# Performance work log

Measured on AMD Instinct MI355X. Metric: run time of the kernel, lower is better.

## Reference

```python
import jax, jax.numpy as jnp
import numpy as np

B, C, L = 8, 512, 8192
H = 8  # head_count
DK = C // H  # head key channels
DV = C // H  # head value channels


def setup_inputs() -> dict:
    key = jax.random.key(0)
    ks = jax.random.split(key, 10)
    s = 1.0 / np.sqrt(C)
    return {
        "input_": jax.random.normal(ks[0], (B, C, L), jnp.float32),
        "context_": jax.random.normal(ks[1], (B, C, L), jnp.float32),
        "Wk": jax.random.normal(ks[2], (C, C), jnp.float32) * s,
        "bk": jax.random.normal(ks[3], (C,), jnp.float32) * 0.01,
        "Wq": jax.random.normal(ks[4], (C, C), jnp.float32) * s,
        "bq": jax.random.normal(ks[5], (C,), jnp.float32) * 0.01,
        "Wv": jax.random.normal(ks[6], (C, C), jnp.float32) * s,
        "bv": jax.random.normal(ks[7], (C,), jnp.float32) * 0.01,
        "Wr": jax.random.normal(ks[8], (C, C), jnp.float32) * s,
        "br": jax.random.normal(ks[9], (C,), jnp.float32) * 0.01,
    }


def _proj(W, b, x):
    # 1x1 Conv1d == channel matmul: [O,C] x [B,C,L] -> [B,O,L]
    return jnp.einsum('oc,bcl->bol', W, x) + b[None, :, None]


def reference(input_, context_, Wk, bk, Wq, bq, Wv, bv, Wr, br):
    b, _, l = input_.shape
    keys = _proj(Wk, bk, context_).reshape(b, H, DK, l)
    queries = _proj(Wq, bq, input_).reshape(b, H, DK, l)
    values = _proj(Wv, bv, context_).reshape(b, H, DV, l)
    # per-head: softmax(K) over sequence, softmax(Q) over head-key channels
    k = jax.nn.softmax(keys, axis=3)
    q = jax.nn.softmax(queries, axis=2)
    # context = K @ V^T : [b,h,dk,dv]
    ctx = jnp.einsum('bhkl,bhvl->bhkv', k, values)
    # attended = context^T @ Q : [b,h,dv,l]
    att = jnp.einsum('bhkv,bhkl->bhvl', ctx, q).reshape(b, H * DV, l)
    return _proj(Wr, br, att) + input_
```

## Files before the change

### kernel.cpp

```cpp
#include <hip/hip_runtime.h>

#define NB 8
#define NC 512
#define NL 8192
#define NH 8
#define ND 64

typedef float f32x4 __attribute__((ext_vector_type(4)));
typedef __bf16 bf16x8 __attribute__((ext_vector_type(8)));
typedef unsigned int u32x4 __attribute__((ext_vector_type(4)));

__device__ __forceinline__ unsigned short f2bf(float f) {
    unsigned u = __builtin_bit_cast(unsigned, f);
    u += 0x7fffu + ((u >> 16) & 1u);
    return (unsigned short)(u >> 16);
}
__device__ __forceinline__ float bf2f(unsigned short s) {
    unsigned u = ((unsigned)s) << 16;
    return __builtin_bit_cast(float, u);
}
__device__ __forceinline__ float bf2f_lo(unsigned w) {
    return __builtin_bit_cast(float, w << 16);
}
__device__ __forceinline__ float bf2f_hi(unsigned w) {
    return __builtin_bit_cast(float, w & 0xffff0000u);
}
__device__ __forceinline__ bf16x8 frag_from_u32x4(u32x4 v) {
    return __builtin_bit_cast(bf16x8, v);
}
__device__ __forceinline__ bf16x8 ld_frag_lds(const unsigned short* p) {
    const unsigned* q = (const unsigned*)p;
    u32x4 v = { q[0], q[1], q[2], q[3] };
    return frag_from_u32x4(v);
}
__device__ __forceinline__ bf16x8 ld_frag_g16(const unsigned short* p) {
    return frag_from_u32x4(*(const u32x4*)p);
}

__global__ __launch_bounds__(256) void cvt_w_kernel(const float* __restrict__ s,
                                                    unsigned short* __restrict__ d, int n) {
    int i = blockIdx.x * 256 + threadIdx.x;
    if (i < n) d[i] = f2bf(s[i]);
}

__global__ __launch_bounds__(256) void zero_kernel(float* __restrict__ p, int n) {
    int i = blockIdx.x * 256 + threadIdx.x;
    if (i < n) p[i] = 0.f;
}

__global__ __launch_bounds__(256) void concat_bias_kernel(const float* __restrict__ a,
                                                          const float* __restrict__ b,
                                                          float* __restrict__ d) {
    int i = blockIdx.x * 256 + threadIdx.x;
    d[i] = (i < NC) ? a[i] : b[i - NC];
}

template<int MT, bool XBF, bool RESID, bool PERB, bool QSM>
__global__ __launch_bounds__(256) void gemm_kernel(
    const unsigned short* __restrict__ Wb,
    const void* __restrict__ Xv,
    const float* __restrict__ bias,
    const float* __restrict__ resid,
    void* __restrict__ Yv)
{
    const int bx = blockIdx.x;
    const int g  = bx >> 3;
    const int mt = g % MT;
    const int nt = (g / MT) * 8 + (bx & 7);
    const int b  = blockIdx.y;
    const int t  = threadIdx.x;
    const int wave = t >> 6, lane = t & 63;
    const int m0 = mt * 128, n0 = nt * 128;
    const int wm = (wave & 1) * 64, wn = (wave >> 1) * 64;
    const int OC = MT * 128;

    __shared__ alignas(16) unsigned short lA[128][34];
    __shared__ alignas(16) unsigned short lX[128][34];

    f32x4 acc[4][4] = {};

    const float* Xf = (const float*)Xv;
    const unsigned short* Xh = (const unsigned short*)Xv;
    const size_t xbase = (size_t)b * NC * NL;
    const unsigned short* Wp = Wb + (PERB ? (size_t)b * NC * NC : 0);

    for (int k0 = 0; k0 < NC; k0 += 32) {
        {
            int id = t;
            #pragma unroll
            for (int it = 0; it < 2; ++it, id += 256) {
                const int r = id >> 2, s = id & 3;
                u32x4 v = *(const u32x4*)(Wp + (size_t)(m0 + r) * NC + k0 + s * 8);
                unsigned* p = (unsigned*)&lA[r][s * 8];
                p[0] = v.x; p[1] = v.y; p[2] = v.z; p[3] = v.w;
            }
        }
        if constexpr (!XBF) {
            #pragma unroll
            for (int it = 0; it < 16; ++it) {
                const int kr = it * 2 + (t >> 7);
                const int l  = t & 127;
                lX[l][kr] = f2bf(Xf[xbase + (size_t)(k0 + kr) * NL + n0 + l]);
            }
        } else {
            #pragma unroll
            for (int it = 0; it < 8; ++it) {
                const int kr = it * 4 + (t >> 6);
                const int l2 = (t & 63) * 2;
                unsigned v = *(const unsigned*)(Xh + xbase + (size_t)(k0 + kr) * NL + n0 + l2);
                lX[l2][kr]     = (unsigned short)(v & 0xffffu);
                lX[l2 + 1][kr] = (unsigned short)(v >> 16);
            }
        }
        __syncthreads();

        const int koff = (lane >> 4) * 8;
        bf16x8 af[4], bfx[4];
        #pragma unroll
        for (int i = 0; i < 4; ++i)
            af[i] = ld_frag_lds(&lA[wm + i * 16 + (lane & 15)][koff]);
        #pragma unroll
        for (int j = 0; j < 4; ++j)
            bfx[j] = ld_frag_lds(&lX[wn + j * 16 + (lane & 15)][koff]);
        #pragma unroll
        for (int i = 0; i < 4; ++i)
            #pragma unroll
            for (int j = 0; j < 4; ++j)
                acc[i][j] = __builtin_amdgcn_mfma_f32_16x16x32_bf16(af[i], bfx[j], acc[i][j], 0, 0, 0);
        __syncthreads();
    }

    const int col = lane & 15, row0 = (lane >> 4) * 4;

    if constexpr (QSM) {
        #pragma unroll
        for (int i = 0; i < 4; ++i)
            #pragma unroll
            for (int r = 0; r < 4; ++r) {
                const float bo = bias[m0 + wm + i * 16 + row0 + r];
                #pragma unroll
                for (int j = 0; j < 4; ++j) acc[i][j][r] += bo;
            }
        float inv[4];
        #pragma unroll
        for (int j = 0; j < 4; ++j) {
            float m = -1e30f;
            #pragma unroll
            for (int i = 0; i < 4; ++i)
                #pragma unroll
                for (int r = 0; r < 4; ++r) m = fmaxf(m, acc[i][j][r]);
            m = fmaxf(m, __shfl_xor(m, 16));
            m = fmaxf(m, __shfl_xor(m, 32));
            float s = 0.f;
            #pragma unroll
            for (int i = 0; i < 4; ++i)
                #pragma unroll
                for (int r = 0; r < 4; ++r) {
                    const float e = __expf(acc[i][j][r] - m);
                    acc[i][j][r] = e;
                    s += e;
                }
            s += __shfl_xor(s, 16);
            s += __shfl_xor(s, 32);
            inv[j] = 1.0f / s;
        }
        unsigned short* Y = (unsigned short*)Yv;
        #pragma unroll
        for (int i = 0; i < 4; ++i)
            #pragma unroll
            for (int r = 0; r < 4; ++r) {
                const int o = m0 + wm + i * 16 + row0 + r;
                const size_t rb = (size_t)b * OC * NL + (size_t)o * NL + n0 + wn;
                #pragma unroll
                for (int j = 0; j < 4; ++j)
                    Y[rb + j * 16 + col] = f2bf(acc[i][j][r] * inv[j]);
            }
    } else {
        #pragma unroll
        for (int i = 0; i < 4; ++i) {
            #pragma unroll
            for (int r = 0; r < 4; ++r) {
                const int o = m0 + wm + i * 16 + row0 + r;
                const float bo = bias[o];
                const size_t rb = (size_t)b * OC * NL + (size_t)o * NL + n0 + wn;
                if constexpr (RESID) {
                    float* Y = (float*)Yv;
                    #pragma unroll
                    for (int j = 0; j < 4; ++j) {
                        const size_t idx = rb + j * 16 + col;
                        Y[idx] = acc[i][j][r] + bo + resid[idx];
                    }
                } else {
                    unsigned short* Y = (unsigned short*)Yv;
                    #pragma unroll
                    for (int j = 0; j < 4; ++j)
                        Y[rb + j * 16 + col] = f2bf(acc[i][j][r] + bo);
                }
            }
        }
    }
}

__global__ __launch_bounds__(256) void softmax_rows(unsigned short* __restrict__ KV) {
    const int row = blockIdx.x;
    const int t = threadIdx.x;
    const int wave = t >> 6, lane = t & 63;
    unsigned short* p = KV + ((size_t)(row >> 9) * 2 * NC + (row & 511)) * NL;

    float v[32];
    float mx = -1e30f;
    #pragma unroll
    for (int i = 0; i < 4; ++i) {
        u32x4 raw = *(const u32x4*)(p + (size_t)(i * 256 + t) * 8);
        #pragma unroll
        for (int d = 0; d < 4; ++d) {
            unsigned w = raw[d];
            v[i * 8 + d * 2]     = bf2f_lo(w);
            v[i * 8 + d * 2 + 1] = bf2f_hi(w);
        }
        #pragma unroll
        for (int j = 0; j < 8; ++j) mx = fmaxf(mx, v[i * 8 + j]);
    }
    #pragma unroll
    for (int off = 32; off > 0; off >>= 1) mx = fmaxf(mx, __shfl_down(mx, off));
    __shared__ float red[16];
    if (lane == 0) red[wave] = mx;
    __syncthreads();
    mx = fmaxf(fmaxf(red[0], red[1]), fmaxf(red[2], red[3]));

    float s = 0.f;
    #pragma unroll
    for (int i = 0; i < 32; ++i) { v[i] = __expf(v[i] - mx); s += v[i]; }
    #pragma unroll
    for (int off = 32; off > 0; off >>= 1) s += __shfl_down(s, off);
    if (lane == 0) red[8 + wave] = s;
    __syncthreads();
    s = red[8] + red[9] + red[10] + red[11];
    const float inv = 1.0f / s;

    #pragma unroll
    for (int i = 0; i < 4; ++i) {
        u32x4 outw;
        #pragma unroll
        for (int d = 0; d < 4; ++d) {
            unsigned lo = f2bf(v[i * 8 + d * 2] * inv);
            unsigned hi = f2bf(v[i * 8 + d * 2 + 1] * inv);
            outw[d] = lo | (hi << 16);
        }
        *(u32x4*)(p + (size_t)(i * 256 + t) * 8) = outw;
    }
}

__global__ __launch_bounds__(256) void ctx_kernel(
    const unsigned short* __restrict__ KV,
    float* __restrict__ ctx)
{
    const int bh = blockIdx.x;
    const int sp = blockIdx.y;
    const int t = threadIdx.x;
    const int wave = t >> 6, lane = t & 63;
    const int b = bh >> 3, h = bh & 7;
    const size_t base_k = ((size_t)b * 2 * NC + h * ND) * NL;
    const size_t base_v = base_k + (size_t)NC * NL;
    const int i = wave * 16 + (lane & 15);
    const int koff = (lane >> 4) * 8;
    const unsigned short* Ka = KV + base_k + (size_t)i * NL + koff;

    f32x4 acc[4] = {};
    const int l0 = sp * (NL / 16);
    for (int l = l0; l < l0 + (NL / 16); l += 32) {
        bf16x8 a = ld_frag_g16(Ka + l);
        #pragma unroll
        for (int j = 0; j < 4; ++j) {
            bf16x8 bv = ld_frag_g16(KV + base_v + (size_t)(j * 16 + (lane & 15)) * NL + l + koff);
            acc[j] = __builtin_amdgcn_mfma_f32_16x16x32_bf16(a, bv, acc[j], 0, 0, 0);
        }
    }
    const int col = lane & 15, row0 = (lane >> 4) * 4;
    #pragma unroll
    for (int j = 0; j < 4; ++j)
        #pragma unroll
        for (int r = 0; r < 4; ++r)
            atomicAdd(&ctx[(size_t)bh * (ND * ND) + (size_t)(wave * 16 + row0 + r) * ND + j * 16 + col],
                      acc[j][r]);
}

__global__ __launch_bounds__(512) void fold_kernel(
    const unsigned short* __restrict__ Wrb,
    const float* __restrict__ ctxb,
    unsigned short* __restrict__ Mb)
{
    const int bh = blockIdx.x;
    const int b = bh >> 3, h = bh & 7;
    const int t = threadIdx.x;
    const int wave = t >> 6, lane = t & 63;

    __shared__ unsigned short lc[64 * 66];
    const float* cs = ctxb + (size_t)bh * (ND * ND);
    #pragma unroll
    for (int it = 0; it < 8; ++it) {
        int i = it * 512 + t;
        lc[(i >> 6) * 66 + (i & 63)] = f2bf(cs[i]);
    }
    __syncthreads();

    const int koff = (lane >> 4) * 8;
    f32x4 acc[4][4] = {};
    #pragma unroll
    for (int kk = 0; kk < 64; kk += 32) {
        bf16x8 af[4], bfx[4];
        #pragma unroll
        for (int i = 0; i < 4; ++i)
            af[i] = ld_frag_g16(Wrb + (size_t)(wave * 64 + i * 16 + (lane & 15)) * NC
                                + h * ND + kk + koff);
        #pragma unroll
        for (int j = 0; j < 4; ++j)
            bfx[j] = ld_frag_lds(&lc[(j * 16 + (lane & 15)) * 66 + kk + koff]);
        #pragma unroll
        for (int i = 0; i < 4; ++i)
            #pragma unroll
            for (int j = 0; j < 4; ++j)
                acc[i][j] = __builtin_amdgcn_mfma_f32_16x16x32_bf16(af[i], bfx[j], acc[i][j], 0, 0, 0);
    }

    const int col = lane & 15, row0 = (lane >> 4) * 4;
    #pragma unroll
    for (int i = 0; i < 4; ++i)
        #pragma unroll
        for (int r = 0; r < 4; ++r) {
            const int o = wave * 64 + i * 16 + row0 + r;
            #pragma unroll
            for (int j = 0; j < 4; ++j)
                Mb[(size_t)b * NC * NC + (size_t)o * NC + h * ND + j * 16 + col]
                    = f2bf(acc[i][j][r]);
        }
}

extern "C" void kernel_launch(void* const* d_in, const int* in_sizes, int n_in,
                              void* d_out, int out_size, void* d_ws, size_t ws_size,
                              hipStream_t stream) {
    (void)in_sizes; (void)n_in; (void)out_size; (void)ws_size;
    const float* input_   = (const float*)d_in[0];
    const float* context_ = (const float*)d_in[1];
    const float* Wk = (const float*)d_in[2];
    const float* bk = (const float*)d_in[3];
    const float* Wq = (const float*)d_in[4];
    const float* bq = (const float*)d_in[5];
    const float* Wv = (const float*)d_in[6];
    const float* bv = (const float*)d_in[7];
    const float* Wr = (const float*)d_in[8];
    const float* br = (const float*)d_in[9];
    float* out = (float*)d_out;

    char* ws = (char*)d_ws;
    unsigned short* Wkvb = (unsigned short*)ws;
    unsigned short* Wqb  = Wkvb + 2 * NC * NC;
    unsigned short* Wrb  = Wqb + NC * NC;
    float* bkv  = (float*)(Wrb + NC * NC);
    float* ctxb = bkv + 2 * NC;
    unsigned short* KVp = (unsigned short*)(ctxb + NB * NH * ND * ND);
    unsigned short* Qp  = KVp + (size_t)NB * 2 * NC * NL;
    unsigned short* Mb  = KVp;

    const int wN = NC * NC;
    cvt_w_kernel<<<wN / 256, 256, 0, stream>>>(Wk, Wkvb, wN);
    cvt_w_kernel<<<wN / 256, 256, 0, stream>>>(Wv, Wkvb + wN, wN);
    cvt_w_kernel<<<wN / 256, 256, 0, stream>>>(Wq, Wqb, wN);
    cvt_w_kernel<<<wN / 256, 256, 0, stream>>>(Wr, Wrb, wN);
    concat_bias_kernel<<<4, 256, 0, stream>>>(bk, bv, bkv);
    zero_kernel<<<(NB * NH * ND * ND) / 256, 256, 0, stream>>>(ctxb, NB * NH * ND * ND);

    gemm_kernel<8, false, false, false, false><<<dim3(64 * 8, NB), 256, 0, stream>>>(
        Wkvb, context_, bkv, nullptr, KVp);
    gemm_kernel<4, false, false, false, true><<<dim3(64 * 4, NB), 256, 0, stream>>>(
        Wqb, input_, bq, nullptr, Qp);

    softmax_rows<<<NB * NC, 256, 0, stream>>>(KVp);
    ctx_kernel<<<dim3(NB * NH, 16), 256, 0, stream>>>(KVp, ctxb);
    fold_kernel<<<NB * NH, 512, 0, stream>>>(Wrb, ctxb, Mb);

    gemm_kernel<4, true, true, true, false><<<dim3(64 * 4, NB), 256, 0, stream>>>(
        Mb, Qp, br, input_, out);
}
```

Before: 725.8 us.

## Pre-transpose activations to bf16 L-major and stage GEMM tiles via direct LDS loads

Adds a transpose-and-convert kernel that writes context and input as bf16 in [L, C] layout, so GEMM X tiles become contiguous 16-byte rows. These tiles and the weight tiles are then loaded with global_load_lds into XOR-swizzled shared memory, replacing the per-element fp32 loads, converts and scalar LDS stores. The Q-softmax GEMM now writes Q transposed, with packed 8-byte stores, so the final GEMM can consume it the same way. The cost is an extra pass over both activations and reuse of the output buffer as scratch for the transposed input.

```diff
diff --git a/kernel.cpp b/kernel.cpp
--- a/kernel.cpp
+++ b/kernel.cpp
@@ -15,10 +15,6 @@
     u += 0x7fffu + ((u >> 16) & 1u);
     return (unsigned short)(u >> 16);
 }
-__device__ __forceinline__ float bf2f(unsigned short s) {
-    unsigned u = ((unsigned)s) << 16;
-    return __builtin_bit_cast(float, u);
-}
 __device__ __forceinline__ float bf2f_lo(unsigned w) {
     return __builtin_bit_cast(float, w << 16);
 }
@@ -35,6 +31,12 @@
 }
 __device__ __forceinline__ bf16x8 ld_frag_g16(const unsigned short* p) {
     return frag_from_u32x4(*(const u32x4*)p);
+}
+
+__device__ __forceinline__ void gload16(const unsigned short* g, unsigned short* l) {
+    __builtin_amdgcn_global_load_lds(
+        (const __attribute__((address_space(1))) unsigned int*)g,
+        (__attribute__((address_space(3))) unsigned int*)l, 16, 0, 0);
 }
 
 __global__ __launch_bounds__(256) void cvt_w_kernel(const float* __restrict__ s,
@@ -55,10 +57,46 @@
     d[i] = (i < NC) ? a[i] : b[i - NC];
 }
 
-template<int MT, bool XBF, bool RESID, bool PERB, bool QSM>
+__device__ __forceinline__ int ltidx(int c, int l) {
+    return c * 64 + ((((l) >> 2) ^ ((c >> 2) & 15)) << 2) + (l & 3);
+}
+__global__ __launch_bounds__(256) void transpose_cvt_kernel(
+    const float* __restrict__ X, unsigned short* __restrict__ Y)
+{
+    const int b = blockIdx.z;
+    const int l0 = blockIdx.x * 64, c0 = blockIdx.y * 64;
+    const int t = threadIdx.x;
+    __shared__ alignas(16) unsigned short lt[64 * 64];
+    const float* Xb = X + (size_t)b * NC * NL;
+    #pragma unroll
+    for (int it = 0; it < 4; ++it) {
+        const int c = it * 16 + (t >> 4), l4 = (t & 15) * 4;
+        f32x4 v = *(const f32x4*)(Xb + (size_t)(c0 + c) * NL + l0 + l4);
+        unsigned lo = f2bf(v.x) | ((unsigned)f2bf(v.y) << 16);
+        unsigned hi = f2bf(v.z) | ((unsigned)f2bf(v.w) << 16);
+        unsigned* p = (unsigned*)&lt[ltidx(c, l4)];
+        p[0] = lo; p[1] = hi;
+    }
+    __syncthreads();
+    unsigned short* Yb = Y + (size_t)b * NL * NC;
+    #pragma unroll
+    for (int it = 0; it < 2; ++it) {
+        const int l = it * 32 + (t >> 3), c8 = (t & 7) * 8;
+        u32x4 o;
+        #pragma unroll
+        for (int d = 0; d < 4; ++d) {
+            unsigned lo = lt[ltidx(c8 + 2 * d, l)];
+            unsigned hi = lt[ltidx(c8 + 2 * d + 1, l)];
+            o[d] = lo | (hi << 16);
+        }
+        *(u32x4*)(Yb + (size_t)(l0 + l) * NC + c0 + c8) = o;
+    }
+}
+
+template<int MT, bool RESID, bool PERB, bool QSMT>
 __global__ __launch_bounds__(256) void gemm_kernel(
     const unsigned short* __restrict__ Wb,
-    const void* __restrict__ Xv,
+    const unsigned short* __restrict__ Xt,
     const float* __restrict__ bias,
     const float* __restrict__ resid,
     void* __restrict__ Yv)
@@ -74,54 +112,38 @@
     const int wm = (wave & 1) * 64, wn = (wave >> 1) * 64;
     const int OC = MT * 128;
 
-    __shared__ alignas(16) unsigned short lA[128][34];
-    __shared__ alignas(16) unsigned short lX[128][34];
+    __shared__ alignas(16) unsigned short lA[128 * 32];
+    __shared__ alignas(16) unsigned short lX[128 * 32];
 
     f32x4 acc[4][4] = {};
 
-    const float* Xf = (const float*)Xv;
-    const unsigned short* Xh = (const unsigned short*)Xv;
-    const size_t xbase = (size_t)b * NC * NL;
     const unsigned short* Wp = Wb + (PERB ? (size_t)b * NC * NC : 0);
+    const unsigned short* Xb = Xt + (size_t)b * NL * NC;
+
+    const int lr = lane & 15, q = lane >> 4;
+    const unsigned aoff = (unsigned)((wm + lr) * 64 + (q ^ (((wm + lr) >> 1) & 3)) * 16);
+    const unsigned boff = (unsigned)((wn + lr) * 64 + (q ^ (((wn + lr) >> 1) & 3)) * 16);
+    const int pb0 = wave * 128;
 
     for (int k0 = 0; k0 < NC; k0 += 32) {
-        {
-            int id = t;
-            #pragma unroll
-            for (int it = 0; it < 2; ++it, id += 256) {
-                const int r = id >> 2, s = id & 3;
-                u32x4 v = *(const u32x4*)(Wp + (size_t)(m0 + r) * NC + k0 + s * 8);
-                unsigned* p = (unsigned*)&lA[r][s * 8];
-                p[0] = v.x; p[1] = v.y; p[2] = v.z; p[3] = v.w;
-            }
-        }
-        if constexpr (!XBF) {
-            #pragma unroll
-            for (int it = 0; it < 16; ++it) {
-                const int kr = it * 2 + (t >> 7);
-                const int l  = t & 127;
-                lX[l][kr] = f2bf(Xf[xbase + (size_t)(k0 + kr) * NL + n0 + l]);
-            }
-        } else {
-            #pragma unroll
-            for (int it = 0; it < 8; ++it) {
-                const int kr = it * 4 + (t >> 6);
-                const int l2 = (t & 63) * 2;
-                unsigned v = *(const unsigned*)(Xh + xbase + (size_t)(k0 + kr) * NL + n0 + l2);
-                lX[l2][kr]     = (unsigned short)(v & 0xffffu);
-                lX[l2 + 1][kr] = (unsigned short)(v >> 16);
-            }
+        #pragma unroll
+        for (int cc = 0; cc < 2; ++cc) {
+            const int pb = pb0 + cc * 64;
+            const int p  = pb + lane;
+            const int r  = p >> 2;
+            const int qq = (p & 3) ^ ((r >> 1) & 3);
+            gload16(Wp + (size_t)(m0 + r) * NC + k0 + qq * 8, &lA[pb * 8]);
+            gload16(Xb + (size_t)(n0 + r) * NC + k0 + qq * 8, &lX[pb * 8]);
         }
         __syncthreads();
 
-        const int koff = (lane >> 4) * 8;
         bf16x8 af[4], bfx[4];
         #pragma unroll
         for (int i = 0; i < 4; ++i)
-            af[i] = ld_frag_lds(&lA[wm + i * 16 + (lane & 15)][koff]);
+            af[i] = frag_from_u32x4(*(const u32x4*)((const char*)lA + aoff + i * 1024));
         #pragma unroll
         for (int j = 0; j < 4; ++j)
-            bfx[j] = ld_frag_lds(&lX[wn + j * 16 + (lane & 15)][koff]);
+            bfx[j] = frag_from_u32x4(*(const u32x4*)((const char*)lX + boff + j * 1024));
         #pragma unroll
         for (int i = 0; i < 4; ++i)
             #pragma unroll
@@ -132,7 +154,7 @@
 
     const int col = lane & 15, row0 = (lane >> 4) * 4;
 
-    if constexpr (QSM) {
+    if constexpr (QSMT) {
         #pragma unroll
         for (int i = 0; i < 4; ++i)
             #pragma unroll
@@ -164,17 +186,19 @@
             s += __shfl_xor(s, 32);
             inv[j] = 1.0f / s;
         }
-        unsigned short* Y = (unsigned short*)Yv;
-        #pragma unroll
-        for (int i = 0; i < 4; ++i)
-            #pragma unroll
-            for (int r = 0; r < 4; ++r) {
-                const int o = m0 + wm + i * 16 + row0 + r;
-                const size_t rb = (size_t)b * OC * NL + (size_t)o * NL + n0 + wn;
-                #pragma unroll
-                for (int j = 0; j < 4; ++j)
-                    Y[rb + j * 16 + col] = f2bf(acc[i][j][r] * inv[j]);
+        unsigned short* Yq = (unsigned short*)Yv;
+        #pragma unroll
+        for (int j = 0; j < 4; ++j) {
+            const size_t rowb = (size_t)b * NL * NC + (size_t)(n0 + wn + j * 16 + col) * NC;
+            #pragma unroll
+            for (int i = 0; i < 4; ++i) {
+                const int o0 = m0 + wm + i * 16 + row0;
+                unsigned lo = f2bf(acc[i][j][0] * inv[j]) | ((unsigned)f2bf(acc[i][j][1] * inv[j]) << 16);
+                unsigned hi = f2bf(acc[i][j][2] * inv[j]) | ((unsigned)f2bf(acc[i][j][3] * inv[j]) << 16);
+                *(unsigned long long*)(Yq + rowb + o0) =
+                    (unsigned long long)lo | ((unsigned long long)hi << 32);
             }
+        }
     } else {
         #pragma unroll
         for (int i = 0; i < 4; ++i) {
@@ -359,8 +383,9 @@
     float* bkv  = (float*)(Wrb + NC * NC);
     float* ctxb = bkv + 2 * NC;
     unsigned short* KVp = (unsigned short*)(ctxb + NB * NH * ND * ND);
-    unsigned short* Qp  = KVp + (size_t)NB * 2 * NC * NL;
+    unsigned short* R2  = KVp + (size_t)NB * 2 * NC * NL;
     unsigned short* Mb  = KVp;
+    unsigned short* Xt_in = (unsigned short*)d_out;
 
     const int wN = NC * NC;
     cvt_w_kernel<<<wN / 256, 256, 0, stream>>>(Wk, Wkvb, wN);
@@ -370,15 +395,20 @@
     concat_bias_kernel<<<4, 256, 0, stream>>>(bk, bv, bkv);
     zero_kernel<<<(NB * NH * ND * ND) / 256, 256, 0, stream>>>(ctxb, NB * NH * ND * ND);
 
-    gemm_kernel<8, false, false, false, false><<<dim3(64 * 8, NB), 256, 0, stream>>>(
-        Wkvb, context_, bkv, nullptr, KVp);
-    gemm_kernel<4, false, false, false, true><<<dim3(64 * 4, NB), 256, 0, stream>>>(
-        Wqb, input_, bq, nullptr, Qp);
+    transpose_cvt_kernel<<<dim3(NL / 64, NC / 64, NB), 256, 0, stream>>>(context_, R2);
+
+    gemm_kernel<8, false, false, false><<<dim3(64 * 8, NB), 256, 0, stream>>>(
+        Wkvb, R2, bkv, nullptr, KVp);
+
+    transpose_cvt_kernel<<<dim3(NL / 64, NC / 64, NB), 256, 0, stream>>>(input_, Xt_in);
+
+    gemm_kernel<4, false, false, true><<<dim3(64 * 4, NB), 256, 0, stream>>>(
+        Wqb, Xt_in, bq, nullptr, R2);
 
     softmax_rows<<<NB * NC, 256, 0, stream>>>(KVp);
     ctx_kernel<<<dim3(NB * NH, 16), 256, 0, stream>>>(KVp, ctxb);
     fold_kernel<<<NB * NH, 512, 0, stream>>>(Wrb, ctxb, Mb);
 
-    gemm_kernel<4, true, true, true, false><<<dim3(64 * 4, NB), 256, 0, stream>>>(
-        Mb, Qp, br, input_, out);
-}
+    gemm_kernel<4, true, true, false><<<dim3(64 * 4, NB), 256, 0, stream>>>(
+        Mb, R2, br, input_, out);
+}
```

New measurement: 654.6 us. -9.8%, faster.
